# Performance work log

Measured on AMD Instinct MI355X. Metric: run time of the kernel, lower is better.

## Reference

```python
import jax, jax.numpy as jnp
import numpy as np

V, E, H, F, A, L = 32000, 256, 512, 512, 256, 49  # vocab, embed, hidden, feature, attn, n_locations
B, T = 64, 32


def setup_inputs() -> dict:
    key = jax.random.key(0)
    ks = jax.random.split(key, 16)
    s = lambda k, sh: (jax.random.normal(k, sh, jnp.float32) * 0.02)
    embedding = s(ks[0], (V, E)).at[0].set(0.0)  # padding_idx=0 row zeroed
    return dict(
        image_feats=jax.random.normal(ks[1], (B, L, F), jnp.float32),
        caption_in=jax.random.randint(ks[2], (B, T), 0, V, dtype=jnp.int32),
        embedding=embedding,
        W_init_h=s(ks[3], (F, H)), b_init_h=jnp.zeros((H,), jnp.float32),
        W_init_c=s(ks[4], (F, H)), b_init_c=jnp.zeros((H,), jnp.float32),
        W_feat=s(ks[5], (F, A)), b_feat=jnp.zeros((A,), jnp.float32),
        W_hid=s(ks[6], (H, A)), b_hid=jnp.zeros((A,), jnp.float32),
        W_score=s(ks[7], (A,)), b_score=jnp.zeros((), jnp.float32),
        W_ih=s(ks[8], (E + F, 4 * H)), b_ih=jnp.zeros((4 * H,), jnp.float32),
        W_hh=s(ks[9], (H, 4 * H)), b_hh=jnp.zeros((4 * H,), jnp.float32),
        W_out=s(ks[10], (H, V)), b_out=jnp.zeros((V,), jnp.float32),
    )


def reference(image_feats, caption_in, embedding,
              W_init_h, b_init_h, W_init_c, b_init_c,
              W_feat, b_feat, W_hid, b_hid, W_score, b_score,
              W_ih, b_ih, W_hh, b_hh, W_out, b_out):
    # init_hidden_state: mean over spatial locations -> two linears
    mean_feats = image_feats.mean(axis=1)                      # (B, F)
    h0 = mean_feats @ W_init_h + b_init_h                      # (B, H)
    c0 = mean_feats @ W_init_c + b_init_c                      # (B, H)
    embs = embedding[caption_in]                               # (B, T, E); dropout = identity (eval)
    feat_proj = image_feats @ W_feat + b_feat                  # (B, L, A) - invariant over t, precompute

    def step(carry, emb_t):
        h, c = carry
        # additive attention
        energy = jnp.tanh(feat_proj + (h @ W_hid + b_hid)[:, None, :])   # (B, L, A)
        scores = energy @ W_score + b_score                              # (B, L)
        alpha = jax.nn.softmax(scores, axis=1)                           # (B, L)
        context = jnp.einsum('bl,blf->bf', alpha, image_feats)           # (B, F)
        # LSTMCell (torch gate order i, f, g, o)
        x = jnp.concatenate([emb_t, context], axis=1)                    # (B, E+F)
        gates = x @ W_ih + b_ih + h @ W_hh + b_hh                        # (B, 4H)
        i, f, g, o = jnp.split(gates, 4, axis=1)
        i = jax.nn.sigmoid(i); f = jax.nn.sigmoid(f); o = jax.nn.sigmoid(o)
        c_new = f * c + i * jnp.tanh(g)
        h_new = o * jnp.tanh(c_new)
        logits_t = h_new @ W_out + b_out                                 # (B, V); dropout = identity
        return (h_new, c_new), (logits_t, alpha)

    _, (logits, alphas) = jax.lax.scan(step, (h0, c0), jnp.swapaxes(embs, 0, 1))
    predictions = jnp.swapaxes(logits, 0, 1)   # (B, T, V)
    all_alphas = jnp.swapaxes(alphas, 0, 1)    # (B, T, L)
    return predictions, all_alphas
```

## Files before the change

### kernel.cpp

```cpp
#include <hip/hip_runtime.h>
#include <hip/hip_bf16.h>

typedef _Float16 f16;
typedef _Float16 f16x8 __attribute__((ext_vector_type(8)));
typedef _Float16 f16x4 __attribute__((ext_vector_type(4)));
typedef _Float16 f16x2 __attribute__((ext_vector_type(2)));
typedef float f32x4 __attribute__((ext_vector_type(4)));
typedef unsigned long long ull;

#define B_ 64
#define T_ 32
#define L_ 49
#define F_ 512
#define H_ 512
#define A_ 256
#define E_ 256
#define V_ 32000
#define G4 2048
#define NG 64
#define NLOG 125
#define SLOT 16

#define ALOAD32(p)     __hip_atomic_load((const unsigned*)(p), __ATOMIC_RELAXED, __HIP_MEMORY_SCOPE_AGENT)
#define ASTORE32(p, v) __hip_atomic_store((unsigned*)(p), (v), __ATOMIC_RELAXED, __HIP_MEMORY_SCOPE_AGENT)
#define ASTORE64(p, v) __hip_atomic_store((ull*)(p), (v), __ATOMIC_RELAXED, __HIP_MEMORY_SCOPE_AGENT)

#if defined(__has_builtin)
#if __has_builtin(__builtin_amdgcn_fdot2)
#define HAS_FDOT2 1
#endif
#endif

#define NB_TC0 (64 * 24)
#define NB_TC1 (64 * 16)
#define NB_Q   128
#define NB_CVT 1568
#define NB_EMB 2048
#define NB_INIT 64
#define NB_FP  196

__device__ void dev_tcvt(const float* __restrict__ x, f16* __restrict__ y,
                         int R, int C, int bx, int by, char* smem) {
    float (*ls)[33] = (float(*)[33])smem;
    int c0 = bx * 32, r0 = by * 32;
    int tid = threadIdx.x;
    int rr = tid >> 3, cs = (tid & 7) * 4;
    float4 v = *(const float4*)&x[(size_t)(r0 + rr) * C + c0 + cs];
    ls[rr][cs] = v.x; ls[rr][cs + 1] = v.y; ls[rr][cs + 2] = v.z; ls[rr][cs + 3] = v.w;
    __syncthreads();
    int cr = tid >> 3, rs = (tid & 7) * 4;
    f16x4 o = {(f16)ls[rs][cr], (f16)ls[rs + 1][cr], (f16)ls[rs + 2][cr], (f16)ls[rs + 3][cr]};
    *(f16x4*)&y[(size_t)(c0 + cr) * R + r0 + rs] = o;
}

__global__ __launch_bounds__(256) void k_prep(
    const float* __restrict__ image_feats, const int* __restrict__ caption,
    const float* __restrict__ embedding,
    const float* __restrict__ W_init_h, const float* __restrict__ b_init_h,
    const float* __restrict__ W_init_c, const float* __restrict__ b_init_c,
    const float* __restrict__ W_feat, const float* __restrict__ b_feat,
    const float* __restrict__ W_hid, const float* __restrict__ W_ih,
    const float* __restrict__ W_hh,
    f16* __restrict__ feats16, f16* __restrict__ embs16,
    f16* __restrict__ WihT, f16* __restrict__ WhhT,
    f16* __restrict__ Whidp,
    f16* __restrict__ hslab, float* __restrict__ c_cur,
    float* __restrict__ featproj) {
    __shared__ __align__(16) char smem[32768];
    int bid = blockIdx.x, tid = threadIdx.x;
    int r = bid;
    if (r < NB_TC0) { dev_tcvt(W_ih, WihT, E_ + F_, G4, r % 64, r / 64, smem); return; }
    r -= NB_TC0;
    if (r < NB_TC1) { dev_tcvt(W_hh, WhhT, H_, G4, r % 64, r / 64, smem); return; }
    r -= NB_TC1;
    if (r < NB_Q) {
        int k4 = r;
        f16 buf[4];
#pragma unroll
        for (int j = 0; j < 4; ++j) buf[j] = (f16)W_hid[(size_t)(4 * k4 + j) * 256 + tid];
        *(f16x4*)&Whidp[((size_t)k4 * 256 + tid) * 4] = *(f16x4*)buf;
        return;
    }
    r -= NB_Q;
    if (r < NB_CVT) {
        int i = r * 256 + tid;
        float4 v = ((const float4*)image_feats)[i];
        f16x4 h = {(f16)v.x, (f16)v.y, (f16)v.z, (f16)v.w};
        ((f16x4*)feats16)[i] = h;
        return;
    }
    r -= NB_CVT;
    if (r < NB_EMB) {
        int tok = caption[r];
        embs16[(size_t)r * E_ + tid] = (f16)embedding[(size_t)tok * E_ + tid];
        return;
    }
    r -= NB_EMB;
    if (r < NB_INIT) {
        float* mean = (float*)smem;
        int b = r;
        for (int f = tid; f < F_; f += 256) {
            float s = 0.f;
            for (int l = 0; l < L_; ++l) s += image_feats[((size_t)b * L_ + l) * F_ + f];
            mean[f] = s * (1.f / 49.f);
        }
        __syncthreads();
        for (int h = tid; h < H_; h += 256) {
            float a = b_init_h[h], c = b_init_c[h];
            for (int k = 0; k < F_; ++k) {
                float m = mean[k];
                a += m * W_init_h[k * H_ + h];
                c += m * W_init_c[k * H_ + h];
            }
            hslab[(size_t)b * H_ + h] = (f16)a;
            c_cur[b * H_ + h] = c;
        }
        return;
    }
    r -= NB_INIT;
    {
        float (*fs)[F_] = (float(*)[F_])smem;
        int r0 = r * 16;
        for (int i = tid; i < 16 * F_; i += 256)
            fs[i >> 9][i & 511] = image_feats[(size_t)r0 * F_ + i];
        __syncthreads();
        float acc[16];
#pragma unroll
        for (int q = 0; q < 16; ++q) acc[q] = 0.f;
        for (int k = 0; k < F_; ++k) {
            float w = W_feat[k * A_ + tid];
#pragma unroll
            for (int q = 0; q < 16; ++q) acc[q] += fs[q][k] * w;
        }
        float bb = b_feat[tid];
#pragma unroll
        for (int q = 0; q < 16; ++q) featproj[(size_t)(r0 + q) * A_ + tid] = acc[q] + bb;
    }
}

struct Smem128 { f16 As[128][40]; f16 Bs[128][40]; };

__global__ __launch_bounds__(256) void k_gemm_emb(
    const f16* __restrict__ A, const f16* __restrict__ Bt,
    f16* __restrict__ Cv, const float* __restrict__ bias0, const float* __restrict__ bias1) {
    __shared__ Smem128 sm;
    int bid = blockIdx.x;
    int mtiles = B_ * T_ / 128;
    int m0 = (bid % mtiles) * 128, n0 = (bid / mtiles) * 128;
    int tid = threadIdx.x, lane = tid & 63, wave = tid >> 6;
    int wr = (wave >> 1) * 64, wc = (wave & 1) * 64;
    int frow = lane & 15, fk = (lane >> 4) * 8;
    int ra = tid >> 2, ka = (tid & 3) * 8;
    f32x4 acc[4][4];
#pragma unroll
    for (int i = 0; i < 4; ++i)
#pragma unroll
        for (int j = 0; j < 4; ++j) { acc[i][j][0]=0.f; acc[i][j][1]=0.f; acc[i][j][2]=0.f; acc[i][j][3]=0.f; }
    for (int k0 = 0; k0 < E_; k0 += 32) {
        f16x8 a0 = *(const f16x8*)&A[(size_t)(m0 + ra) * E_ + k0 + ka];
        f16x8 a1 = *(const f16x8*)&A[(size_t)(m0 + 64 + ra) * E_ + k0 + ka];
        f16x8 b0 = *(const f16x8*)&Bt[(size_t)(n0 + ra) * (E_ + F_) + k0 + ka];
        f16x8 b1 = *(const f16x8*)&Bt[(size_t)(n0 + 64 + ra) * (E_ + F_) + k0 + ka];
        __syncthreads();
        *(f16x8*)&sm.As[ra][ka] = a0;
        *(f16x8*)&sm.As[64 + ra][ka] = a1;
        *(f16x8*)&sm.Bs[ra][ka] = b0;
        *(f16x8*)&sm.Bs[64 + ra][ka] = b1;
        __syncthreads();
        f16x8 av[4], bv[4];
#pragma unroll
        for (int i = 0; i < 4; ++i) {
            av[i] = *(f16x8*)&sm.As[wr + i * 16 + frow][fk];
            bv[i] = *(f16x8*)&sm.Bs[wc + i * 16 + frow][fk];
        }
#pragma unroll
        for (int mi = 0; mi < 4; ++mi)
#pragma unroll
            for (int ni = 0; ni < 4; ++ni)
                acc[mi][ni] = __builtin_amdgcn_mfma_f32_16x16x32_f16(av[mi], bv[ni], acc[mi][ni], 0, 0, 0);
    }
    int rq = (lane >> 4) * 4;
#pragma unroll
    for (int mi = 0; mi < 4; ++mi)
#pragma unroll
        for (int ni = 0; ni < 4; ++ni) {
            int cc = n0 + wc + ni * 16 + frow;
            float badd = bias0[cc] + bias1[cc];
#pragma unroll
            for (int r = 0; r < 4; ++r) {
                int rr = m0 + wr + mi * 16 + rq + r;
                Cv[((size_t)rr * 512 + (cc & 511)) * 4 + (cc >> 9)] =
                    (f16)(acc[mi][ni][r] + badd);
            }
        }
}

struct GateSm {
    float fp[L_][A_];
    unsigned fe[L_ * 256];
    float ea[A_];
    float ws[A_];
    float sc[64];
    float alpha[64];
    unsigned hL[256];
};
struct GemmSm {
    f16 w[32][512];
    f16 w2[32][512];
    union {
        f16 hs[64][512];
        f16 hwT16[64][40];
    } u;
};
struct LogSm { f16 hs[128][512]; };

__device__ __forceinline__ void wait_n(const unsigned* flags, int n, unsigned target) {
    int tid = threadIdx.x;
    if (tid < n) {
        const unsigned* p = flags + tid * SLOT;
        while (ALOAD32(p) < target) __builtin_amdgcn_s_sleep(1);
    }
    asm volatile("" ::: "memory");
    __syncthreads();
}

__device__ __forceinline__ void wait_n_slow(const unsigned* flags, int n, unsigned target) {
    int tid = threadIdx.x;
    if (tid < n) {
        const unsigned* p = flags + tid * SLOT;
        while (ALOAD32(p) < target) __builtin_amdgcn_s_sleep(8);
    }
    asm volatile("" ::: "memory");
    __syncthreads();
}

__device__ __forceinline__ float sigm(float x) { return 1.f / (1.f + __expf(-x)); }
__device__ __forceinline__ float tanh_f(float x) { return 1.f - 2.f / (1.f + __expf(2.f * x)); }

__global__ __launch_bounds__(256, 1) void k_steps(
    const f16* __restrict__ WhhT, const f16* __restrict__ WihT,
    const f16* __restrict__ Whidp,
    const float* __restrict__ featproj, const f16* __restrict__ feats16,
    const float* __restrict__ b_hid,
    const float* __restrict__ W_score, const float* __restrict__ b_score,
    const f16* __restrict__ embP, const float* __restrict__ c_cur,
    f16* __restrict__ hslab, f16* __restrict__ ctxslab, f16* __restrict__ hwcslab,
    const float* __restrict__ W_out, f16* __restrict__ WoutT,
    const float* __restrict__ b_out,
    float* __restrict__ preds, float* __restrict__ out_alpha,
    unsigned* __restrict__ gateflag, unsigned* __restrict__ ctxflag,
    unsigned* __restrict__ gemmflag) {
    __shared__ __align__(16) char smraw[sizeof(LogSm)];
    int bid = blockIdx.x, tid = threadIdx.x;

    if (bid < 64) {
        int b = bid;
        GateSm* S = (GateSm*)smraw;
        for (int i = tid; i < L_ * A_; i += 256)
            ((float*)S->fp)[i] = featproj[(size_t)b * L_ * A_ + i];
        {
            const f16x8* src = (const f16x8*)(feats16 + (size_t)b * L_ * F_);
            f16x8* dst = (f16x8*)S->fe;
            for (int i = tid; i < L_ * F_ / 8; i += 256) dst[i] = src[i];
        }
        S->ws[tid] = W_score[tid];
        float bhid_r = b_hid[tid];
        float bsc = b_score[0];
        S->hL[tid] = ((const unsigned*)hslab)[(size_t)b * 256 + tid];
        float cs0 = c_cur[b * H_ + 2 * tid], cs1 = c_cur[b * H_ + 2 * tid + 1];
        const f16x4* wp4 = (const f16x4*)Whidp;
        int wv = tid >> 6, ln = tid & 63;
        __syncthreads();

        for (int t = 0; t < T_; ++t) {
            {
                float acc = bhid_r;
#pragma unroll 16
                for (int k4 = 0; k4 < 128; ++k4) {
                    union { f16x4 v; f16x2 p[2]; } w;
                    w.v = wp4[(size_t)k4 * 256 + tid];
                    union { unsigned u; f16x2 v; } h0, h1;
                    h0.u = S->hL[2 * k4];
                    h1.u = S->hL[2 * k4 + 1];
#ifdef HAS_FDOT2
                    acc = __builtin_amdgcn_fdot2(w.p[0], h0.v, acc, false);
                    acc = __builtin_amdgcn_fdot2(w.p[1], h1.v, acc, false);
#else
                    acc += (float)w.p[0].x * (float)h0.v.x + (float)w.p[0].y * (float)h0.v.y;
                    acc += (float)w.p[1].x * (float)h1.v.x + (float)w.p[1].y * (float)h1.v.y;
#endif
                }
                S->ea[tid] = acc;
            }
            __syncthreads();
            for (int l = wv; l < L_; l += 4) {
                float p = 0.f;
#pragma unroll
                for (int q = 0; q < 4; ++q) {
                    int j = ln + q * 64;
                    p += tanh_f(S->fp[l][j] + S->ea[j]) * S->ws[j];
                }
#pragma unroll
                for (int off = 32; off > 0; off >>= 1) p += __shfl_xor(p, off);
                if (ln == 0) S->sc[l] = p;
            }
            __syncthreads();
            if (tid < 64) {
                float v = (tid < L_) ? S->sc[tid] + bsc : -3.4e38f;
                float m = v;
#pragma unroll
                for (int off = 32; off > 0; off >>= 1) m = fmaxf(m, __shfl_xor(m, off));
                float e = (tid < L_) ? __expf(v - m) : 0.f;
                float s = e;
#pragma unroll
                for (int off = 32; off > 0; off >>= 1) s += __shfl_xor(s, off);
                if (tid < L_) {
                    float al = e / s;
                    S->alpha[tid] = al;
                    out_alpha[((size_t)b * T_ + t) * L_ + tid] = al;
                }
            }
            __syncthreads();
            {
                float c0 = 0.f, c1 = 0.f;
#pragma unroll 7
                for (int l = 0; l < L_; ++l) {
                    float a = S->alpha[l];
                    union { unsigned u; f16x2 v; } fv;
                    fv.u = S->fe[l * 256 + tid];
                    c0 += a * (float)fv.v.x;
                    c1 += a * (float)fv.v.y;
                }
                union { f16 h[2]; unsigned u; } pk;
                pk.h[0] = (f16)c0; pk.h[1] = (f16)c1;
                ASTORE32((unsigned*)ctxslab + ((size_t)t * B_ + b) * 256 + tid, pk.u);
            }
            __syncthreads();
            if (tid == 0) ASTORE32(&ctxflag[b * SLOT], (unsigned)(t + 1));
            f16x8 ep = *(const f16x8*)&embP[((size_t)b * T_ + t) * G4 + 8 * tid];
            wait_n(gemmflag, NG, (unsigned)(t + 1));
            {
                f16x8 hw = *(const f16x8*)&hwcslab[((size_t)t * B_ + b) * G4 + 8 * tid];
                float gA[8];
#pragma unroll
                for (int i = 0; i < 8; ++i) gA[i] = (float)hw[i] + (float)ep[i];
                float cn0 = sigm(gA[1]) * cs0 + sigm(gA[0]) * tanh_f(gA[2]);
                float cn1 = sigm(gA[5]) * cs1 + sigm(gA[4]) * tanh_f(gA[6]);
                float hn0 = sigm(gA[3]) * tanh_f(cn0);
                float hn1 = sigm(gA[7]) * tanh_f(cn1);
                cs0 = cn0; cs1 = cn1;
                union { f16 h[2]; unsigned u; } pk;
                pk.h[0] = (f16)hn0; pk.h[1] = (f16)hn1;
                S->hL[tid] = pk.u;
                ASTORE32((unsigned*)hslab + ((size_t)(t + 1) * B_ + b) * 256 + tid, pk.u);
            }
            __syncthreads();
            if (tid == 0)
                ASTORE32(&gateflag[b * SLOT], (unsigned)(t + 2));
        }
    } else if (bid < 64 + NG) {
        int g = bid - 64;
        GemmSm* S = (GemmSm*)smraw;
        for (int i = 0; i < 8; ++i) {
            int idx = i * 256 + tid;
            int r = idx >> 6, ch = idx & 63;
            int cc = (r & 3) * 512 + 8 * g + (r >> 2);
            *(f16x8*)&S->w[r][(ch ^ (r & 7)) * 8] =
                *(const f16x8*)&WhhT[(size_t)cc * 512 + ch * 8];
            *(f16x8*)&S->w2[r][(ch ^ (r & 7)) * 8] =
                *(const f16x8*)&WihT[(size_t)cc * (E_ + F_) + E_ + ch * 8];
        }
        int wvv = tid >> 6, lane = tid & 63;
        int frow = lane & 15, q = lane >> 4, sw = frow & 7, rq = q * 4;
        int mb = (wvv >> 1) * 32, c16 = (wvv & 1) * 16;
        int bo = tid >> 2, cq = (tid & 3) * 8;
        __syncthreads();

        for (int t = 0; t < T_; ++t) {
            if (t) wait_n(gateflag, 64, (unsigned)(t + 1));
            {
                const f16* hsrc = hslab + (size_t)t * B_ * H_;
#pragma unroll
                for (int i = 0; i < 16; ++i) {
                    int idx = i * 256 + tid;
                    int r = idx >> 6, ch = idx & 63;
                    *(f16x8*)&S->u.hs[r][(ch ^ (r & 7)) * 8] =
                        *(const f16x8*)&hsrc[(size_t)r * H_ + ch * 8];
                }
            }
            __syncthreads();
            f32x4 a4[2];
            a4[0][0]=0.f; a4[0][1]=0.f; a4[0][2]=0.f; a4[0][3]=0.f;
            a4[1][0]=0.f; a4[1][1]=0.f; a4[1][2]=0.f; a4[1][3]=0.f;
#pragma unroll
            for (int kk = 0; kk < 16; ++kk) {
                int ch = ((kk * 4 + q) ^ sw) * 8;
                f16x8 bv = *(f16x8*)&S->w[c16 + frow][ch];
                f16x8 av0 = *(f16x8*)&S->u.hs[mb + frow][ch];
                f16x8 av1 = *(f16x8*)&S->u.hs[mb + 16 + frow][ch];
                a4[0] = __builtin_amdgcn_mfma_f32_16x16x32_f16(av0, bv, a4[0], 0, 0, 0);
                a4[1] = __builtin_amdgcn_mfma_f32_16x16x32_f16(av1, bv, a4[1], 0, 0, 0);
            }
            wait_n(ctxflag, 64, (unsigned)(t + 1));
            {
                const f16* csrc = ctxslab + (size_t)t * B_ * F_;
#pragma unroll
                for (int i = 0; i < 16; ++i) {
                    int idx = i * 256 + tid;
                    int r = idx >> 6, ch = idx & 63;
                    *(f16x8*)&S->u.hs[r][(ch ^ (r & 7)) * 8] =
                        *(const f16x8*)&csrc[(size_t)r * F_ + ch * 8];
                }
            }
            __syncthreads();
#pragma unroll
            for (int kk = 0; kk < 16; ++kk) {
                int ch = ((kk * 4 + q) ^ sw) * 8;
                f16x8 bv = *(f16x8*)&S->w2[c16 + frow][ch];
                f16x8 av0 = *(f16x8*)&S->u.hs[mb + frow][ch];
                f16x8 av1 = *(f16x8*)&S->u.hs[mb + 16 + frow][ch];
                a4[0] = __builtin_amdgcn_mfma_f32_16x16x32_f16(av0, bv, a4[0], 0, 0, 0);
                a4[1] = __builtin_amdgcn_mfma_f32_16x16x32_f16(av1, bv, a4[1], 0, 0, 0);
            }
            __syncthreads();
#pragma unroll
            for (int mi = 0; mi < 2; ++mi)
#pragma unroll
                for (int r = 0; r < 4; ++r)
                    S->u.hwT16[mb + mi * 16 + rq + r][c16 + frow] = (f16)a4[mi][r];
            __syncthreads();
            {
                f16* dst = hwcslab + ((size_t)t * B_ + bo) * G4 + 32 * g + cq;
                union { f16 h[4]; ull u; } pk0, pk1;
                *(f16x4*)pk0.h = *(f16x4*)&S->u.hwT16[bo][cq];
                *(f16x4*)pk1.h = *(f16x4*)&S->u.hwT16[bo][cq + 4];
                ASTORE64(dst, pk0.u);
                ASTORE64(dst + 4, pk1.u);
            }
            __syncthreads();
            if (tid == 0)
                ASTORE32(&gemmflag[g * SLOT], (unsigned)(t + 1));
        }
    } else {
        int nt = bid - 64 - NG;
        int n0 = nt * 256;
        LogSm* S = (LogSm*)smraw;
        int wvv = tid >> 6, lane = tid & 63;
        int frow = lane & 15, q = lane >> 4, sw = frow & 7, rq = q * 4;

        {
            float (*ls)[33] = (float(*)[33])smraw;
            int rr = tid >> 3, cs = (tid & 7) * 4;
            int cr = tid >> 3, rs = (tid & 7) * 4;
            for (int c0 = 0; c0 < 256; c0 += 32)
                for (int k0 = 0; k0 < 512; k0 += 32) {
                    float4 v = *(const float4*)&W_out[(size_t)(k0 + rr) * V_ + n0 + c0 + cs];
                    __syncthreads();
                    ls[rr][cs] = v.x; ls[rr][cs + 1] = v.y; ls[rr][cs + 2] = v.z; ls[rr][cs + 3] = v.w;
                    __syncthreads();
                    f16x4 o = {(f16)ls[rs][cr], (f16)ls[rs + 1][cr],
                               (f16)ls[rs + 2][cr], (f16)ls[rs + 3][cr]};
                    *(f16x4*)&WoutT[(size_t)(n0 + c0 + cr) * 512 + k0 + rs] = o;
                }
            __syncthreads();
        }

        for (int tc = 0; tc < T_ / 2; ++tc) {
            wait_n_slow(gateflag, 64, (unsigned)(2 * tc + 3));
            {
                const f16* hsrc = hslab + (size_t)(2 * tc + 1) * B_ * H_;
#pragma unroll
                for (int i = 0; i < 32; ++i) {
                    int idx = i * 256 + tid;
                    int r = idx >> 6, ch = idx & 63;
                    *(f16x8*)&S->hs[r][(ch ^ (r & 7)) * 8] =
                        *(const f16x8*)&hsrc[(size_t)r * H_ + ch * 8];
                }
            }
            __syncthreads();
            f32x4 acc[8][4];
#pragma unroll
            for (int mi = 0; mi < 8; ++mi)
#pragma unroll
                for (int ni = 0; ni < 4; ++ni) { acc[mi][ni][0]=0.f; acc[mi][ni][1]=0.f; acc[mi][ni][2]=0.f; acc[mi][ni][3]=0.f; }
#pragma unroll 2
            for (int kk = 0; kk < 16; ++kk) {
                int ch = ((kk * 4 + q) ^ sw) * 8;
                f16x8 av[8], bv[4];
#pragma unroll
                for (int mi = 0; mi < 8; ++mi)
                    av[mi] = *(f16x8*)&S->hs[mi * 16 + frow][ch];
#pragma unroll
                for (int ni = 0; ni < 4; ++ni)
                    bv[ni] = *(const f16x8*)&WoutT[(size_t)(n0 + wvv * 64 + ni * 16 + frow) * 512 + kk * 32 + q * 8];
#pragma unroll
                for (int mi = 0; mi < 8; ++mi)
#pragma unroll
                    for (int ni = 0; ni < 4; ++ni)
                        acc[mi][ni] = __builtin_amdgcn_mfma_f32_16x16x32_f16(av[mi], bv[ni], acc[mi][ni], 0, 0, 0);
            }
#pragma unroll
            for (int ni = 0; ni < 4; ++ni) {
                int cc = n0 + wvv * 64 + ni * 16 + frow;
                float badd = b_out[cc];
#pragma unroll
                for (int mi = 0; mi < 8; ++mi)
#pragma unroll
                    for (int r = 0; r < 4; ++r) {
                        int rr = mi * 16 + rq + r;
                        int tt = 2 * tc + (rr >> 6), bb2 = rr & 63;
                        preds[((size_t)bb2 * T_ + tt) * V_ + cc] = acc[mi][ni][r] + badd;
                    }
            }
            __syncthreads();
        }
    }
}

extern "C" void kernel_launch(void* const* d_in, const int* in_sizes, int n_in,
                              void* d_out, int out_size, void* d_ws, size_t ws_size,
                              hipStream_t stream) {
    const float* image_feats = (const float*)d_in[0];
    const int*   caption     = (const int*)d_in[1];
    const float* embedding   = (const float*)d_in[2];
    const float* W_init_h    = (const float*)d_in[3];
    const float* b_init_h    = (const float*)d_in[4];
    const float* W_init_c    = (const float*)d_in[5];
    const float* b_init_c    = (const float*)d_in[6];
    const float* W_feat      = (const float*)d_in[7];
    const float* b_feat      = (const float*)d_in[8];
    const float* W_hid       = (const float*)d_in[9];
    const float* b_hid       = (const float*)d_in[10];
    const float* W_score     = (const float*)d_in[11];
    const float* b_score     = (const float*)d_in[12];
    const float* W_ih        = (const float*)d_in[13];
    const float* b_ih        = (const float*)d_in[14];
    const float* W_hh        = (const float*)d_in[15];
    const float* b_hh        = (const float*)d_in[16];
    const float* W_out       = (const float*)d_in[17];
    const float* b_out       = (const float*)d_in[18];

    float* preds = (float*)d_out;
    float* out_alpha = preds + (size_t)B_ * T_ * V_;

    size_t off = 0;
    char* base = (char*)d_ws;
    auto carve = [&](size_t bytes) {
        void* p = base + off;
        off += (bytes + 255) & ~(size_t)255;
        return p;
    };
    f16* embP       = (f16*)carve((size_t)B_ * T_ * G4 * 2);
    float* featproj = (float*)carve((size_t)B_ * L_ * A_ * 4);
    float* c_cur    = (float*)carve((size_t)B_ * H_ * 4);
    f16* hslab      = (f16*)carve((size_t)(T_ + 1) * B_ * H_ * 2);
    f16* ctxslab    = (f16*)carve((size_t)T_ * B_ * F_ * 2);
    f16* hwcslab    = (f16*)carve((size_t)T_ * B_ * G4 * 2);
    unsigned* flags = (unsigned*)carve((64 + 64 + NG) * SLOT * 4);
    f16* feats16    = (f16*)carve((size_t)B_ * L_ * F_ * 2);
    f16* embs16     = (f16*)carve((size_t)B_ * T_ * E_ * 2);
    f16* WihT       = (f16*)carve((size_t)G4 * (E_ + F_) * 2);
    f16* WhhT       = (f16*)carve((size_t)G4 * H_ * 2);
    f16* WoutT      = (f16*)carve((size_t)V_ * H_ * 2);
    f16* Whidp      = (f16*)carve((size_t)H_ * A_ * 2);
    unsigned* gateflag = flags;
    unsigned* ctxflag  = flags + 64 * SLOT;
    unsigned* gemmflag = flags + 128 * SLOT;
    (void)ws_size; (void)in_sizes; (void)n_in; (void)out_size;

    {
        int nb = NB_TC0 + NB_TC1 + NB_Q + NB_CVT + NB_EMB + NB_INIT + NB_FP;
        hipLaunchKernelGGL(k_prep, dim3(nb), dim3(256), 0, stream,
                           image_feats, caption, embedding,
                           W_init_h, b_init_h, W_init_c, b_init_c,
                           W_feat, b_feat, W_hid, W_ih, W_hh,
                           feats16, embs16, WihT, WhhT, Whidp,
                           hslab, c_cur, featproj);
    }
    hipLaunchKernelGGL(k_gemm_emb, dim3((B_ * T_ / 128) * (G4 / 128)), dim3(256), 0, stream,
                       embs16, WihT, embP, b_ih, b_hh);
    hipMemsetAsync(flags, 0, (64 + 64 + NG) * SLOT * 4, stream);
    hipLaunchKernelGGL(k_steps, dim3(64 + NG + NLOG), dim3(256), 0, stream,
                       WhhT, WihT, Whidp, featproj, feats16, b_hid,
                       W_score, b_score, embP, c_cur,
                       hslab, ctxslab, hwcslab,
                       W_out, WoutT, b_out, preds, out_alpha,
                       gateflag, ctxflag, gemmflag);
}
```

Measured before the change: 626.4 us.

## Fuse weight conversion and embedding GEMM into prep and persistent kernels

Drops the separate fp32→fp16 transpose passes for W_ih/W_hh, the image-feature and embedding conversions, and the standalone embedding GEMM kernel. The embedding gather and fp16 cast now happen inside a GEMM tile section of k_prep, and the persistent step kernel reads fp32 weights and image features and converts them while filling shared memory. This removes a kernel launch and several global round trips of intermediate fp16 copies. In exchange, conversion work moves into the latency-critical persistent kernel's setup, and the scalar transposed LDS stores may cause bank conflicts.

Measured after the change: 624.3 us. About the same (-0.3%).

```diff
diff --git a/kernel.cpp b/kernel.cpp
--- a/kernel.cpp
+++ b/kernel.cpp
@@ -31,27 +31,12 @@
 #endif
 #endif
 
-#define NB_TC0 (64 * 24)
-#define NB_TC1 (64 * 16)
-#define NB_Q   128
-#define NB_CVT 1568
-#define NB_EMB 2048
+#define NB_EMBG 256
+#define NB_Q    128
 #define NB_INIT 64
-#define NB_FP  196
-
-__device__ void dev_tcvt(const float* __restrict__ x, f16* __restrict__ y,
-                         int R, int C, int bx, int by, char* smem) {
-    float (*ls)[33] = (float(*)[33])smem;
-    int c0 = bx * 32, r0 = by * 32;
-    int tid = threadIdx.x;
-    int rr = tid >> 3, cs = (tid & 7) * 4;
-    float4 v = *(const float4*)&x[(size_t)(r0 + rr) * C + c0 + cs];
-    ls[rr][cs] = v.x; ls[rr][cs + 1] = v.y; ls[rr][cs + 2] = v.z; ls[rr][cs + 3] = v.w;
-    __syncthreads();
-    int cr = tid >> 3, rs = (tid & 7) * 4;
-    f16x4 o = {(f16)ls[rs][cr], (f16)ls[rs + 1][cr], (f16)ls[rs + 2][cr], (f16)ls[rs + 3][cr]};
-    *(f16x4*)&y[(size_t)(c0 + cr) * R + r0 + rs] = o;
-}
+#define NB_FP   196
+
+struct Smem128 { f16 As[128][40]; f16 Bs[128][40]; };
 
 __global__ __launch_bounds__(256) void k_prep(
     const float* __restrict__ image_feats, const int* __restrict__ caption,
@@ -60,19 +45,81 @@
     const float* __restrict__ W_init_c, const float* __restrict__ b_init_c,
     const float* __restrict__ W_feat, const float* __restrict__ b_feat,
     const float* __restrict__ W_hid, const float* __restrict__ W_ih,
-    const float* __restrict__ W_hh,
-    f16* __restrict__ feats16, f16* __restrict__ embs16,
-    f16* __restrict__ WihT, f16* __restrict__ WhhT,
-    f16* __restrict__ Whidp,
+    const float* __restrict__ b_ih, const float* __restrict__ b_hh,
+    f16* __restrict__ embP, f16* __restrict__ Whidp,
     f16* __restrict__ hslab, float* __restrict__ c_cur,
     float* __restrict__ featproj) {
     __shared__ __align__(16) char smem[32768];
     int bid = blockIdx.x, tid = threadIdx.x;
     int r = bid;
-    if (r < NB_TC0) { dev_tcvt(W_ih, WihT, E_ + F_, G4, r % 64, r / 64, smem); return; }
-    r -= NB_TC0;
-    if (r < NB_TC1) { dev_tcvt(W_hh, WhhT, H_, G4, r % 64, r / 64, smem); return; }
-    r -= NB_TC1;
+    if (r < NB_EMBG) {
+        Smem128* sm = (Smem128*)smem;
+        int mtiles = B_ * T_ / 128;
+        int m0 = (r % mtiles) * 128, n0 = (r / mtiles) * 128;
+        int lane = tid & 63, wave = tid >> 6;
+        int wr = (wave >> 1) * 64, wc = (wave & 1) * 64;
+        int frow = lane & 15, fk = (lane >> 4) * 8;
+        int ra = tid >> 2, ka = (tid & 3) * 8;
+        int kb = tid >> 3, nb = (tid & 7) * 16;
+        int tok0 = caption[m0 + ra], tok1 = caption[m0 + 64 + ra];
+        f32x4 acc[4][4];
+#pragma unroll
+        for (int i = 0; i < 4; ++i)
+#pragma unroll
+            for (int j = 0; j < 4; ++j) { acc[i][j][0]=0.f; acc[i][j][1]=0.f; acc[i][j][2]=0.f; acc[i][j][3]=0.f; }
+        for (int k0 = 0; k0 < E_; k0 += 32) {
+            float4 e00 = *(const float4*)&embedding[(size_t)tok0 * E_ + k0 + ka];
+            float4 e01 = *(const float4*)&embedding[(size_t)tok0 * E_ + k0 + ka + 4];
+            float4 e10 = *(const float4*)&embedding[(size_t)tok1 * E_ + k0 + ka];
+            float4 e11 = *(const float4*)&embedding[(size_t)tok1 * E_ + k0 + ka + 4];
+            const float* wrow = W_ih + (size_t)(k0 + kb) * G4 + n0 + nb;
+            float4 w0 = *(const float4*)wrow;
+            float4 w1 = *(const float4*)(wrow + 4);
+            float4 w2 = *(const float4*)(wrow + 8);
+            float4 w3 = *(const float4*)(wrow + 12);
+            __syncthreads();
+            {
+                f16x8 a0 = {(f16)e00.x,(f16)e00.y,(f16)e00.z,(f16)e00.w,
+                            (f16)e01.x,(f16)e01.y,(f16)e01.z,(f16)e01.w};
+                f16x8 a1 = {(f16)e10.x,(f16)e10.y,(f16)e10.z,(f16)e10.w,
+                            (f16)e11.x,(f16)e11.y,(f16)e11.z,(f16)e11.w};
+                *(f16x8*)&sm->As[ra][ka] = a0;
+                *(f16x8*)&sm->As[64 + ra][ka] = a1;
+                float wv[16] = {w0.x,w0.y,w0.z,w0.w, w1.x,w1.y,w1.z,w1.w,
+                                w2.x,w2.y,w2.z,w2.w, w3.x,w3.y,w3.z,w3.w};
+#pragma unroll
+                for (int j = 0; j < 16; ++j) sm->Bs[nb + j][kb] = (f16)wv[j];
+            }
+            __syncthreads();
+            f16x8 av[4], bv[4];
+#pragma unroll
+            for (int i = 0; i < 4; ++i) {
+                av[i] = *(f16x8*)&sm->As[wr + i * 16 + frow][fk];
+                bv[i] = *(f16x8*)&sm->Bs[wc + i * 16 + frow][fk];
+            }
+#pragma unroll
+            for (int mi = 0; mi < 4; ++mi)
+#pragma unroll
+                for (int ni = 0; ni < 4; ++ni)
+                    acc[mi][ni] = __builtin_amdgcn_mfma_f32_16x16x32_f16(av[mi], bv[ni], acc[mi][ni], 0, 0, 0);
+        }
+        int rq = (lane >> 4) * 4;
+#pragma unroll
+        for (int mi = 0; mi < 4; ++mi)
+#pragma unroll
+            for (int ni = 0; ni < 4; ++ni) {
+                int cc = n0 + wc + ni * 16 + frow;
+                float badd = b_ih[cc] + b_hh[cc];
+#pragma unroll
+                for (int rr2 = 0; rr2 < 4; ++rr2) {
+                    int rr = m0 + wr + mi * 16 + rq + rr2;
+                    embP[((size_t)rr * 512 + (cc & 511)) * 4 + (cc >> 9)] =
+                        (f16)(acc[mi][ni][rr2] + badd);
+                }
+            }
+        return;
+    }
+    r -= NB_EMBG;
     if (r < NB_Q) {
         int k4 = r;
         f16 buf[4];
@@ -82,20 +129,6 @@
         return;
     }
     r -= NB_Q;
-    if (r < NB_CVT) {
-        int i = r * 256 + tid;
-        float4 v = ((const float4*)image_feats)[i];
-        f16x4 h = {(f16)v.x, (f16)v.y, (f16)v.z, (f16)v.w};
-        ((f16x4*)feats16)[i] = h;
-        return;
-    }
-    r -= NB_CVT;
-    if (r < NB_EMB) {
-        int tok = caption[r];
-        embs16[(size_t)r * E_ + tid] = (f16)embedding[(size_t)tok * E_ + tid];
-        return;
-    }
-    r -= NB_EMB;
     if (r < NB_INIT) {
         float* mean = (float*)smem;
         int b = r;
@@ -136,63 +169,6 @@
 #pragma unroll
         for (int q = 0; q < 16; ++q) featproj[(size_t)(r0 + q) * A_ + tid] = acc[q] + bb;
     }
-}
-
-struct Smem128 { f16 As[128][40]; f16 Bs[128][40]; };
-
-__global__ __launch_bounds__(256) void k_gemm_emb(
-    const f16* __restrict__ A, const f16* __restrict__ Bt,
-    f16* __restrict__ Cv, const float* __restrict__ bias0, const float* __restrict__ bias1) {
-    __shared__ Smem128 sm;
-    int bid = blockIdx.x;
-    int mtiles = B_ * T_ / 128;
-    int m0 = (bid % mtiles) * 128, n0 = (bid / mtiles) * 128;
-    int tid = threadIdx.x, lane = tid & 63, wave = tid >> 6;
-    int wr = (wave >> 1) * 64, wc = (wave & 1) * 64;
-    int frow = lane & 15, fk = (lane >> 4) * 8;
-    int ra = tid >> 2, ka = (tid & 3) * 8;
-    f32x4 acc[4][4];
-#pragma unroll
-    for (int i = 0; i < 4; ++i)
-#pragma unroll
-        for (int j = 0; j < 4; ++j) { acc[i][j][0]=0.f; acc[i][j][1]=0.f; acc[i][j][2]=0.f; acc[i][j][3]=0.f; }
-    for (int k0 = 0; k0 < E_; k0 += 32) {
-        f16x8 a0 = *(const f16x8*)&A[(size_t)(m0 + ra) * E_ + k0 + ka];
-        f16x8 a1 = *(const f16x8*)&A[(size_t)(m0 + 64 + ra) * E_ + k0 + ka];
-        f16x8 b0 = *(const f16x8*)&Bt[(size_t)(n0 + ra) * (E_ + F_) + k0 + ka];
-        f16x8 b1 = *(const f16x8*)&Bt[(size_t)(n0 + 64 + ra) * (E_ + F_) + k0 + ka];
-        __syncthreads();
-        *(f16x8*)&sm.As[ra][ka] = a0;
-        *(f16x8*)&sm.As[64 + ra][ka] = a1;
-        *(f16x8*)&sm.Bs[ra][ka] = b0;
-        *(f16x8*)&sm.Bs[64 + ra][ka] = b1;
-        __syncthreads();
-        f16x8 av[4], bv[4];
-#pragma unroll
-        for (int i = 0; i < 4; ++i) {
-            av[i] = *(f16x8*)&sm.As[wr + i * 16 + frow][fk];
-            bv[i] = *(f16x8*)&sm.Bs[wc + i * 16 + frow][fk];
-        }
-#pragma unroll
-        for (int mi = 0; mi < 4; ++mi)
-#pragma unroll
-            for (int ni = 0; ni < 4; ++ni)
-                acc[mi][ni] = __builtin_amdgcn_mfma_f32_16x16x32_f16(av[mi], bv[ni], acc[mi][ni], 0, 0, 0);
-    }
-    int rq = (lane >> 4) * 4;
-#pragma unroll
-    for (int mi = 0; mi < 4; ++mi)
-#pragma unroll
-        for (int ni = 0; ni < 4; ++ni) {
-            int cc = n0 + wc + ni * 16 + frow;
-            float badd = bias0[cc] + bias1[cc];
-#pragma unroll
-            for (int r = 0; r < 4; ++r) {
-                int rr = m0 + wr + mi * 16 + rq + r;
-                Cv[((size_t)rr * 512 + (cc & 511)) * 4 + (cc >> 9)] =
-                    (f16)(acc[mi][ni][r] + badd);
-            }
-        }
 }
 
 struct GateSm {
@@ -223,7 +199,6 @@
     asm volatile("" ::: "memory");
     __syncthreads();
 }
-
 __device__ __forceinline__ void wait_n_slow(const unsigned* flags, int n, unsigned target) {
     int tid = threadIdx.x;
     if (tid < n) {
@@ -238,9 +213,9 @@
 __device__ __forceinline__ float tanh_f(float x) { return 1.f - 2.f / (1.f + __expf(2.f * x)); }
 
 __global__ __launch_bounds__(256, 1) void k_steps(
-    const f16* __restrict__ WhhT, const f16* __restrict__ WihT,
+    const float* __restrict__ W_hh, const float* __restrict__ W_ih,
     const f16* __restrict__ Whidp,
-    const float* __restrict__ featproj, const f16* __restrict__ feats16,
+    const float* __restrict__ featproj, const float* __restrict__ image_feats,
     const float* __restrict__ b_hid,
     const float* __restrict__ W_score, const float* __restrict__ b_score,
     const f16* __restrict__ embP, const float* __restrict__ c_cur,
@@ -259,9 +234,13 @@
         for (int i = tid; i < L_ * A_; i += 256)
             ((float*)S->fp)[i] = featproj[(size_t)b * L_ * A_ + i];
         {
-            const f16x8* src = (const f16x8*)(feats16 + (size_t)b * L_ * F_);
-            f16x8* dst = (f16x8*)S->fe;
-            for (int i = tid; i < L_ * F_ / 8; i += 256) dst[i] = src[i];
+            const float2* src = (const float2*)(image_feats + (size_t)b * L_ * F_);
+            for (int i = tid; i < L_ * 256; i += 256) {
+                float2 v = src[i];
+                union { f16 h[2]; unsigned u; } pk;
+                pk.h[0] = (f16)v.x; pk.h[1] = (f16)v.y;
+                S->fe[i] = pk.u;
+            }
         }
         S->ws[tid] = W_score[tid];
         float bhid_r = b_hid[tid];
@@ -361,14 +340,26 @@
     } else if (bid < 64 + NG) {
         int g = bid - 64;
         GemmSm* S = (GemmSm*)smraw;
-        for (int i = 0; i < 8; ++i) {
-            int idx = i * 256 + tid;
-            int r = idx >> 6, ch = idx & 63;
-            int cc = (r & 3) * 512 + 8 * g + (r >> 2);
-            *(f16x8*)&S->w[r][(ch ^ (r & 7)) * 8] =
-                *(const f16x8*)&WhhT[(size_t)cc * 512 + ch * 8];
-            *(f16x8*)&S->w2[r][(ch ^ (r & 7)) * 8] =
-                *(const f16x8*)&WihT[(size_t)cc * (E_ + F_) + E_ + ch * 8];
+        for (int rowbase = 0; rowbase < 512; rowbase += 256) {
+            int k = rowbase + tid;
+            const float* wh = W_hh + (size_t)k * G4 + 8 * g;
+            const float* wi = W_ih + (size_t)(E_ + k) * G4 + 8 * g;
+            int ch = k >> 3, j = k & 7;
+#pragma unroll
+            for (int q = 0; q < 4; ++q) {
+                float4 v0 = *(const float4*)(wh + q * 512);
+                float4 v1 = *(const float4*)(wh + q * 512 + 4);
+                float4 u0 = *(const float4*)(wi + q * 512);
+                float4 u1 = *(const float4*)(wi + q * 512 + 4);
+                float vv[8] = {v0.x,v0.y,v0.z,v0.w, v1.x,v1.y,v1.z,v1.w};
+                float uu[8] = {u0.x,u0.y,u0.z,u0.w, u1.x,u1.y,u1.z,u1.w};
+#pragma unroll
+                for (int d = 0; d < 8; ++d) {
+                    int r = d * 4 + q;
+                    S->w[r][((ch ^ (r & 7)) << 3) + j]  = (f16)vv[d];
+                    S->w2[r][((ch ^ (r & 7)) << 3) + j] = (f16)uu[d];
+                }
+            }
         }
         int wvv = tid >> 6, lane = tid & 63;
         int frow = lane & 15, q = lane >> 4, sw = frow & 7, rq = q * 4;
@@ -557,10 +548,6 @@
     f16* ctxslab    = (f16*)carve((size_t)T_ * B_ * F_ * 2);
     f16* hwcslab    = (f16*)carve((size_t)T_ * B_ * G4 * 2);
     unsigned* flags = (unsigned*)carve((64 + 64 + NG) * SLOT * 4);
-    f16* feats16    = (f16*)carve((size_t)B_ * L_ * F_ * 2);
-    f16* embs16     = (f16*)carve((size_t)B_ * T_ * E_ * 2);
-    f16* WihT       = (f16*)carve((size_t)G4 * (E_ + F_) * 2);
-    f16* WhhT       = (f16*)carve((size_t)G4 * H_ * 2);
     f16* WoutT      = (f16*)carve((size_t)V_ * H_ * 2);
     f16* Whidp      = (f16*)carve((size_t)H_ * A_ * 2);
     unsigned* gateflag = flags;
@@ -568,20 +555,14 @@
     unsigned* gemmflag = flags + 128 * SLOT;
     (void)ws_size; (void)in_sizes; (void)n_in; (void)out_size;
 
-    {
-        int nb = NB_TC0 + NB_TC1 + NB_Q + NB_CVT + NB_EMB + NB_INIT + NB_FP;
-        hipLaunchKernelGGL(k_prep, dim3(nb), dim3(256), 0, stream,
-                           image_feats, caption, embedding,
-                           W_init_h, b_init_h, W_init_c, b_init_c,
-                           W_feat, b_feat, W_hid, W_ih, W_hh,
-                           feats16, embs16, WihT, WhhT, Whidp,
-                           hslab, c_cur, featproj);
-    }
-    hipLaunchKernelGGL(k_gemm_emb, dim3((B_ * T_ / 128) * (G4 / 128)), dim3(256), 0, stream,
-                       embs16, WihT, embP, b_ih, b_hh);
     hipMemsetAsync(flags, 0, (64 + 64 + NG) * SLOT * 4, stream);
+    hipLaunchKernelGGL(k_prep, dim3(NB_EMBG + NB_Q + NB_INIT + NB_FP), dim3(256), 0, stream,
+                       image_feats, caption, embedding,
+                       W_init_h, b_init_h, W_init_c, b_init_c,
+                       W_feat, b_feat, W_hid, W_ih, b_ih, b_hh,
+                       embP, Whidp, hslab, c_cur, featproj);
     hipLaunchKernelGGL(k_steps, dim3(64 + NG + NLOG), dim3(256), 0, stream,
-                       WhhT, WihT, Whidp, featproj, feats16, b_hid,
+                       W_hh, W_ih, Whidp, featproj, image_feats, b_hid,
                        W_score, b_score, embP, c_cur,
                        hslab, ctxslab, hwcslab,
                        W_out, WoutT, b_out, preds, out_alpha,
```
